# Optimization experiments

Measured on AMD Instinct MI355X. Metric: run time of the kernel, lower is better.

Reference implementation:

```python
import jax, jax.numpy as jnp
import numpy as np

B, S, D, H = 8, 1024, 1024, 16
HD = D // H  # head_dim = 64


def setup_inputs() -> dict:
    key = jax.random.key(0)
    ks = jax.random.split(key, 5)
    scale = 1.0 / np.sqrt(D)
    return {
        "x": jax.random.normal(ks[0], (B, S, D), dtype=jnp.float32),
        "wq": jax.random.normal(ks[1], (D, D), dtype=jnp.float32) * scale,
        "wk": jax.random.normal(ks[2], (D, D), dtype=jnp.float32) * scale,
        "wv": jax.random.normal(ks[3], (D, D), dtype=jnp.float32) * scale,
        "wo": jax.random.normal(ks[4], (D, D), dtype=jnp.float32) * scale,
    }


def reference(x, wq, wk, wv, wo):
    b, s, d = x.shape
    # nn.Linear: y = x @ W.T  (weights stored [out, in])
    q = (x @ wq.T).reshape(b, s, H, HD).transpose(0, 2, 1, 3)  # [b,h,s,hd]
    k = (x @ wk.T).reshape(b, s, H, HD).transpose(0, 2, 1, 3)
    v = (x @ wv.T).reshape(b, s, H, HD).transpose(0, 2, 1, 3)
    scores = jnp.einsum("bhqd,bhkd->bhqk", q, k) / jnp.sqrt(jnp.float32(HD))
    attn = jax.nn.softmax(scores, axis=-1)  # dropout p=0.0 -> identity
    out = jnp.einsum("bhqk,bhkd->bhqd", attn, v)
    out = out.transpose(0, 2, 1, 3).reshape(b, s, d)
    return out @ wo.T
```

## Files before the change

kernel.cpp:

```cpp
#include <hip/hip_runtime.h>
#include <hip/hip_bf16.h>
#include <math.h>

#define BB 8
#define SS 1024
#define DD 1024
#define HH 16
#define HDIM 64
#define MM (BB * SS)
#define QSCALE 0.1803368801111204f

typedef __attribute__((ext_vector_type(8))) short s8v;
typedef __attribute__((ext_vector_type(4))) short s4v;
typedef __attribute__((ext_vector_type(4))) float f4v;

#define GLD16(g, l)                                                            \
  __builtin_amdgcn_global_load_lds(                                            \
      (const __attribute__((address_space(1))) void*)(g),                      \
      (__attribute__((address_space(3))) void*)(l), 16, 0, 0)

__device__ __forceinline__ unsigned short bf16_ru(float f) {
  return (unsigned short)((__float_as_uint(f) + 0x8000u) >> 16);
}

__device__ __forceinline__ unsigned bf16_pack2(float f0, float f1) {
#if __has_builtin(__builtin_amdgcn_perm)
  unsigned a = __float_as_uint(f0) + 0x8000u;
  unsigned b = __float_as_uint(f1) + 0x8000u;
  return __builtin_amdgcn_perm(b, a, 0x07060302u);
#else
  return (unsigned)bf16_ru(f0) | ((unsigned)bf16_ru(f1) << 16);
#endif
}

__device__ __forceinline__ float fast_exp2(float x) {
  return __builtin_amdgcn_exp2f(x);
}

__global__ void cast_all(const float* __restrict__ x, const float* __restrict__ wq,
                         const float* __restrict__ wk, const float* __restrict__ wv,
                         const float* __restrict__ wo, __hip_bfloat16* __restrict__ xb,
                         __hip_bfloat16* __restrict__ wqkvb,
                         __hip_bfloat16* __restrict__ wob) {
  int blk = blockIdx.x;
  const float* src;
  __hip_bfloat16* dst;
  int base;
  if (blk < 2048) {
    src = x; dst = xb; base = blk * 4096;
  } else if (blk < 2304) {
    src = wq; dst = wqkvb; base = (blk - 2048) * 4096;
  } else if (blk < 2560) {
    src = wk; dst = wqkvb + (1 << 20); base = (blk - 2304) * 4096;
  } else if (blk < 2816) {
    src = wv; dst = wqkvb + (2 << 20); base = (blk - 2560) * 4096;
  } else {
    src = wo; dst = wob; base = (blk - 2816) * 4096;
  }
#pragma unroll
  for (int it = 0; it < 4; ++it) {
    int idx = base + it * 1024 + threadIdx.x * 4;
    float4 f = *(const float4*)&src[idx];
    *(uint2*)&dst[idx] = uint2{bf16_pack2(f.x, f.y), bf16_pack2(f.z, f.w)};
  }
}

template <int MODE>
__global__ __launch_bounds__(256, (MODE == 0 ? 4 : 3)) void gemm_bt(
    const __hip_bfloat16* __restrict__ A, const __hip_bfloat16* __restrict__ Bm,
    float* __restrict__ Cf, __hip_bfloat16* __restrict__ Qo,
    __hip_bfloat16* __restrict__ Ko, __hip_bfloat16* __restrict__ Vt) {
  __shared__ __hip_bfloat16 smem[2][128 * 64];
  __hip_bfloat16* sA = smem[0];
  __hip_bfloat16* sB = smem[1];

  const int tid = threadIdx.x;
  const int wave = tid >> 6;
  const int lane = tid & 63;
  const int l15 = lane & 15;
  const int quad = lane >> 4;
  const int c8 = lane & 7;
  const int r8 = lane >> 3;

  constexpr int GX = (MODE == 0) ? 16 : 8;
  constexpr int NWG = GX * 64;
  const int id = blockIdx.y * GX + blockIdx.x;
  const int nid = (id & 7) * (NWG / 8) + (id >> 3);
  const int m0 = (nid / GX) * 128;
  const int n0 = (nid % GX) * 128;

  const int wm = (wave >> 1) * 64;
  const int wn = (wave & 1) * 64;

  f4v acc[4][4];
#pragma unroll
  for (int i = 0; i < 4; ++i)
#pragma unroll
    for (int j = 0; j < 4; ++j) acc[i][j] = {0.f, 0.f, 0.f, 0.f};

  for (int kt = 0; kt < DD / 64; ++kt) {
    const int k0 = kt * 64;
    __syncthreads();
#pragma unroll
    for (int r = 0; r < 4; ++r) {
      int rb = r * 32 + wave * 8;
      int row = rb + r8;
      int scol = (c8 ^ (row & 7)) * 8;
      GLD16(A + (size_t)(m0 + row) * DD + k0 + scol, &sA[rb * 64]);
      GLD16(Bm + (size_t)(n0 + row) * DD + k0 + scol, &sB[rb * 64]);
    }
    __syncthreads();

#pragma unroll
    for (int kk = 0; kk < 2; ++kk) {
      s8v af[4], bf[4];
#pragma unroll
      for (int i = 0; i < 4; ++i)
        af[i] = *(const s8v*)&sA[(wm + i * 16 + l15) * 64 +
                                 (((kk * 4 + quad) ^ (l15 & 7)) * 8)];
#pragma unroll
      for (int j = 0; j < 4; ++j)
        bf[j] = *(const s8v*)&sB[(wn + j * 16 + l15) * 64 +
                                 (((kk * 4 + quad) ^ (l15 & 7)) * 8)];
#pragma unroll
      for (int i = 0; i < 4; ++i)
#pragma unroll
        for (int j = 0; j < 4; ++j)
          acc[i][j] = (MODE == 2)
                          ? __builtin_amdgcn_mfma_f32_16x16x32_bf16(af[i], bf[j],
                                                                    acc[i][j], 0, 0, 0)
                          : __builtin_amdgcn_mfma_f32_16x16x32_bf16(bf[j], af[i],
                                                                    acc[i][j], 0, 0, 0);
    }
  }

  if constexpr (MODE == 1) {
#pragma unroll
    for (int i = 0; i < 4; ++i) {
#pragma unroll
      for (int j = 0; j < 4; ++j) {
        const int s_abs = m0 + wm + i * 16 + l15;
        const int col = n0 + wn + j * 16 + quad * 4;
        float4 f4 = {acc[i][j][0], acc[i][j][1], acc[i][j][2], acc[i][j][3]};
        *(float4*)&Cf[(size_t)s_abs * DD + col] = f4;
      }
    }
  } else {
    __syncthreads();
    char* epc = (char*)smem + wave * 8192;
    const float scl = (MODE == 0) ? ((n0 < 1024) ? QSCALE : 1.0f) : 1.0f;
#pragma unroll
    for (int i = 0; i < 4; ++i) {
#pragma unroll
      for (int j = 0; j < 4; ++j) {
        const int r = (MODE == 0 ? i : j) * 16 + l15;
        const int c0 = (MODE == 0 ? j : i) * 16 + quad * 4;
        const int off = r * 128 + (((c0 >> 3) ^ (r & 7)) << 4) + ((c0 & 7) * 2);
        *(uint2*)(epc + off) =
            uint2{bf16_pack2(acc[i][j][0] * scl, acc[i][j][1] * scl),
                  bf16_pack2(acc[i][j][2] * scl, acc[i][j][3] * scl)};
      }
    }
    asm volatile("s_waitcnt lgkmcnt(0)" ::: "memory");
    const int rr8 = lane >> 3;
    const int ch = (lane & 7) ^ rr8;
    if constexpr (MODE == 0) {
      const bool isQ = (n0 < 1024);
      const int h = ((n0 + wn) & 1023) >> 6;
      const int sb = m0 + wm;
      const int b = sb >> 10, s0 = sb & 1023;
      __hip_bfloat16* dst =
          (isQ ? Qo : Ko) + ((size_t)(b * HH + h) * SS + s0) * HDIM;
#pragma unroll
      for (int it = 0; it < 8; ++it) {
        const int r = it * 8 + rr8;
        uint4 vv = *(const uint4*)(epc + r * 128 + ch * 16);
        *(uint4*)&dst[(size_t)r * HDIM + (lane & 7) * 8] = vv;
      }
    } else {
      const int h = ((n0 + wn) & 1023) >> 6;
      const int sb = m0 + wm;
      const int b = sb >> 10, s0 = sb & 1023;
      __hip_bfloat16* dst = Vt + (size_t)(b * HH + h) * HDIM * SS + s0;
#pragma unroll
      for (int it = 0; it < 8; ++it) {
        const int r = it * 8 + rr8;
        uint4 vv = *(const uint4*)(epc + r * 128 + ch * 16);
        *(uint4*)&dst[(size_t)r * SS + (lane & 7) * 8] = vv;
      }
    }
  }
}

#define KPLD 80
__global__ __launch_bounds__(256, 4) void attn_kernel(
    const __hip_bfloat16* __restrict__ Q, const __hip_bfloat16* __restrict__ K,
    const __hip_bfloat16* __restrict__ Vt, __hip_bfloat16* __restrict__ Oout) {
  __shared__ __hip_bfloat16 sK[64 * 64];
  __shared__ __hip_bfloat16 sVt[64 * 64];
  __shared__ unsigned short sP[4 * 32 * KPLD];

  const int tid = threadIdx.x;
  const int wave = tid >> 6;
  const int lane = tid & 63;
  const int l15 = lane & 15;
  const int quad = lane >> 4;
  const int c8 = lane & 7;
  const int r8 = lane >> 3;

  const int bh = blockIdx.x;
  const int q0 = blockIdx.y * 128;
  const size_t head = (size_t)bh * SS * HDIM;

  unsigned short* sPw = &sP[wave * 32 * KPLD];

  s8v qf[2][2];
#pragma unroll
  for (int mf = 0; mf < 2; ++mf) {
    int s = q0 + wave * 32 + mf * 16 + l15;
#pragma unroll
    for (int kk = 0; kk < 2; ++kk)
      qf[mf][kk] = *(const s8v*)&Q[head + (size_t)s * HDIM + kk * 32 + quad * 8];
  }

  s8v onesB;
#pragma unroll
  for (int j = 0; j < 8; ++j) onesB[j] = (short)0x3F80;

  f4v o[2][4];
  f4v lacc[2];
#pragma unroll
  for (int mf = 0; mf < 2; ++mf) {
    lacc[mf] = {0.f, 0.f, 0.f, 0.f};
#pragma unroll
    for (int f = 0; f < 4; ++f) o[mf][f] = {0.f, 0.f, 0.f, 0.f};
  }

  for (int kb = 0; kb < SS / 64; ++kb) {
    __syncthreads();
#pragma unroll
    for (int r = 0; r < 2; ++r) {
      int rb = r * 32 + wave * 8;
      int row = rb + r8;
      int sc8 = (c8 ^ (row & 7)) * 8;
      GLD16(&K[head + (size_t)(kb * 64 + row) * HDIM + sc8], &sK[rb * 64]);
      GLD16(&Vt[head + (size_t)row * SS + kb * 64 + sc8], &sVt[rb * 64]);
    }
    __syncthreads();

    f4v sc[2][4];
#pragma unroll
    for (int mf = 0; mf < 2; ++mf)
#pragma unroll
      for (int f = 0; f < 4; ++f) sc[mf][f] = {0.f, 0.f, 0.f, 0.f};
    __builtin_amdgcn_s_setprio(1);
#pragma unroll
    for (int kk = 0; kk < 2; ++kk) {
#pragma unroll
      for (int f = 0; f < 4; ++f) {
        s8v kf = *(const s8v*)&sK[(f * 16 + l15) * 64 +
                                  (((kk * 4 + quad) ^ (l15 & 7)) * 8)];
#pragma unroll
        for (int mf = 0; mf < 2; ++mf)
          sc[mf][f] =
              __builtin_amdgcn_mfma_f32_16x16x32_bf16(kf, qf[mf][kk], sc[mf][f], 0, 0, 0);
      }
    }
    __builtin_amdgcn_s_setprio(0);

#pragma unroll
    for (int mf = 0; mf < 2; ++mf)
#pragma unroll
      for (int f = 0; f < 4; ++f) {
        float p0 = fast_exp2(sc[mf][f][0]), p1 = fast_exp2(sc[mf][f][1]);
        float p2 = fast_exp2(sc[mf][f][2]), p3 = fast_exp2(sc[mf][f][3]);
        *(uint2*)&sPw[(mf * 16 + l15) * KPLD + f * 16 + quad * 4] =
            uint2{bf16_pack2(p0, p1), bf16_pack2(p2, p3)};
      }

    __builtin_amdgcn_s_setprio(1);
#pragma unroll
    for (int kk = 0; kk < 2; ++kk) {
      s8v pf[2];
#pragma unroll
      for (int mf = 0; mf < 2; ++mf) {
        pf[mf] = *(const s8v*)&sPw[(mf * 16 + l15) * KPLD + kk * 32 + quad * 8];
        lacc[mf] = __builtin_amdgcn_mfma_f32_16x16x32_bf16(pf[mf], onesB, lacc[mf], 0, 0, 0);
      }
#pragma unroll
      for (int f = 0; f < 4; ++f) {
        s8v vf = *(const s8v*)&sVt[(f * 16 + l15) * 64 +
                                   (((kk * 4 + quad) ^ (l15 & 7)) * 8)];
#pragma unroll
        for (int mf = 0; mf < 2; ++mf)
          o[mf][f] =
              __builtin_amdgcn_mfma_f32_16x16x32_bf16(pf[mf], vf, o[mf][f], 0, 0, 0);
      }
    }
    __builtin_amdgcn_s_setprio(0);
  }

  const int b = bh >> 4, h = bh & 15;
#pragma unroll
  for (int mf = 0; mf < 2; ++mf) {
    float rl[4];
#pragma unroll
    for (int r = 0; r < 4; ++r) rl[r] = 1.0f / lacc[mf][r];
#pragma unroll
    for (int f = 0; f < 4; ++f)
#pragma unroll
      for (int r = 0; r < 4; ++r) {
        int srow = q0 + wave * 32 + mf * 16 + quad * 4 + r;
        int col = h * HDIM + f * 16 + l15;
        ((unsigned short*)Oout)[(size_t)(b * SS + srow) * DD + col] =
            bf16_ru(o[mf][f][r] * rl[r]);
      }
  }
}

extern "C" void kernel_launch(void* const* d_in, const int* in_sizes, int n_in,
                              void* d_out, int out_size, void* d_ws, size_t ws_size,
                              hipStream_t stream) {
  const float* x = (const float*)d_in[0];
  const float* wq = (const float*)d_in[1];
  const float* wk = (const float*)d_in[2];
  const float* wv = (const float*)d_in[3];
  const float* wo = (const float*)d_in[4];

  char* ws = (char*)d_ws;
  __hip_bfloat16* xb = (__hip_bfloat16*)(ws);
  __hip_bfloat16* wqkvb = (__hip_bfloat16*)(ws + (16 << 20));
  __hip_bfloat16* wob = (__hip_bfloat16*)(ws + (22 << 20));
  __hip_bfloat16* qh = (__hip_bfloat16*)(ws + (24 << 20));
  __hip_bfloat16* kh = (__hip_bfloat16*)(ws + (40 << 20));
  __hip_bfloat16* vt = (__hip_bfloat16*)(ws + (56 << 20));
  __hip_bfloat16* attnO = (__hip_bfloat16*)(ws + (72 << 20));

  cast_all<<<3072, 256, 0, stream>>>(x, wq, wk, wv, wo, xb, wqkvb, wob);

  gemm_bt<0><<<dim3(16, 64), 256, 0, stream>>>(xb, wqkvb, nullptr, qh, kh, nullptr);
  gemm_bt<2><<<dim3(8, 64), 256, 0, stream>>>(xb, wqkvb + (2 << 20), nullptr,
                                              nullptr, nullptr, vt);

  attn_kernel<<<dim3(BB * HH, SS / 128), 256, 0, stream>>>(qh, kh, vt, attnO);

  gemm_bt<1><<<dim3(8, 64), 256, 0, stream>>>(attnO, wob, (float*)d_out, nullptr,
                                              nullptr, nullptr);
}
```

Before: 226.1 us.

## Fuse V projection into QK GEMM launch and repad attention P buffer

Result: slower. 598.4 us (+164.7%).

```diff
diff --git a/kernel.cpp b/kernel.cpp
--- a/kernel.cpp
+++ b/kernel.cpp
@@ -82,7 +82,7 @@
   const int c8 = lane & 7;
   const int r8 = lane >> 3;
 
-  constexpr int GX = (MODE == 0) ? 16 : 8;
+  constexpr int GX = (MODE == 0) ? 24 : 8;
   constexpr int NWG = GX * 64;
   const int id = blockIdx.y * GX + blockIdx.x;
   const int nid = (id & 7) * (NWG / 8) + (id >> 3);
@@ -91,6 +91,8 @@
 
   const int wm = (wave >> 1) * 64;
   const int wn = (wave & 1) * 64;
+
+  const bool noswap = (MODE == 0) && (n0 >= 2048);
 
   f4v acc[4][4];
 #pragma unroll
@@ -122,15 +124,21 @@
       for (int j = 0; j < 4; ++j)
         bf[j] = *(const s8v*)&sB[(wn + j * 16 + l15) * 64 +
                                  (((kk * 4 + quad) ^ (l15 & 7)) * 8)];
-#pragma unroll
-      for (int i = 0; i < 4; ++i)
-#pragma unroll
-        for (int j = 0; j < 4; ++j)
-          acc[i][j] = (MODE == 2)
-                          ? __builtin_amdgcn_mfma_f32_16x16x32_bf16(af[i], bf[j],
-                                                                    acc[i][j], 0, 0, 0)
-                          : __builtin_amdgcn_mfma_f32_16x16x32_bf16(bf[j], af[i],
-                                                                    acc[i][j], 0, 0, 0);
+      if (noswap) {
+#pragma unroll
+        for (int i = 0; i < 4; ++i)
+#pragma unroll
+          for (int j = 0; j < 4; ++j)
+            acc[i][j] = __builtin_amdgcn_mfma_f32_16x16x32_bf16(af[i], bf[j],
+                                                                acc[i][j], 0, 0, 0);
+      } else {
+#pragma unroll
+        for (int i = 0; i < 4; ++i)
+#pragma unroll
+          for (int j = 0; j < 4; ++j)
+            acc[i][j] = __builtin_amdgcn_mfma_f32_16x16x32_bf16(bf[j], af[i],
+                                                                acc[i][j], 0, 0, 0);
+      }
     }
   }
 
@@ -148,13 +156,14 @@
   } else {
     __syncthreads();
     char* epc = (char*)smem + wave * 8192;
-    const float scl = (MODE == 0) ? ((n0 < 1024) ? QSCALE : 1.0f) : 1.0f;
+    const bool isV = (n0 >= 2048);
+    const float scl = (n0 < 1024) ? QSCALE : 1.0f;
 #pragma unroll
     for (int i = 0; i < 4; ++i) {
 #pragma unroll
       for (int j = 0; j < 4; ++j) {
-        const int r = (MODE == 0 ? i : j) * 16 + l15;
-        const int c0 = (MODE == 0 ? j : i) * 16 + quad * 4;
+        const int r = (isV ? j : i) * 16 + l15;
+        const int c0 = (isV ? i : j) * 16 + quad * 4;
         const int off = r * 128 + (((c0 >> 3) ^ (r & 7)) << 4) + ((c0 & 7) * 2);
         *(uint2*)(epc + off) =
             uint2{bf16_pack2(acc[i][j][0] * scl, acc[i][j][1] * scl),
@@ -164,13 +173,12 @@
     asm volatile("s_waitcnt lgkmcnt(0)" ::: "memory");
     const int rr8 = lane >> 3;
     const int ch = (lane & 7) ^ rr8;
-    if constexpr (MODE == 0) {
-      const bool isQ = (n0 < 1024);
-      const int h = ((n0 + wn) & 1023) >> 6;
-      const int sb = m0 + wm;
-      const int b = sb >> 10, s0 = sb & 1023;
+    const int h = ((n0 + wn) & 1023) >> 6;
+    const int sb = m0 + wm;
+    const int b = sb >> 10, s0 = sb & 1023;
+    if (!isV) {
       __hip_bfloat16* dst =
-          (isQ ? Qo : Ko) + ((size_t)(b * HH + h) * SS + s0) * HDIM;
+          ((n0 < 1024) ? Qo : Ko) + ((size_t)(b * HH + h) * SS + s0) * HDIM;
 #pragma unroll
       for (int it = 0; it < 8; ++it) {
         const int r = it * 8 + rr8;
@@ -178,9 +186,6 @@
         *(uint4*)&dst[(size_t)r * HDIM + (lane & 7) * 8] = vv;
       }
     } else {
-      const int h = ((n0 + wn) & 1023) >> 6;
-      const int sb = m0 + wm;
-      const int b = sb >> 10, s0 = sb & 1023;
       __hip_bfloat16* dst = Vt + (size_t)(b * HH + h) * HDIM * SS + s0;
 #pragma unroll
       for (int it = 0; it < 8; ++it) {
@@ -192,7 +197,7 @@
   }
 }
 
-#define KPLD 80
+#define KPLD 76
 __global__ __launch_bounds__(256, 4) void attn_kernel(
     const __hip_bfloat16* __restrict__ Q, const __hip_bfloat16* __restrict__ K,
     const __hip_bfloat16* __restrict__ Vt, __hip_bfloat16* __restrict__ Oout) {
@@ -284,7 +289,10 @@
       s8v pf[2];
 #pragma unroll
       for (int mf = 0; mf < 2; ++mf) {
-        pf[mf] = *(const s8v*)&sPw[(mf * 16 + l15) * KPLD + kk * 32 + quad * 8];
+        const unsigned short* p = &sPw[(mf * 16 + l15) * KPLD + kk * 32 + quad * 8];
+        s4v lo = *(const s4v*)p;
+        s4v hi = *(const s4v*)(p + 4);
+        pf[mf] = __builtin_shufflevector(lo, hi, 0, 1, 2, 3, 4, 5, 6, 7);
         lacc[mf] = __builtin_amdgcn_mfma_f32_16x16x32_bf16(pf[mf], onesB, lacc[mf], 0, 0, 0);
       }
 #pragma unroll
@@ -338,9 +346,7 @@
 
   cast_all<<<3072, 256, 0, stream>>>(x, wq, wk, wv, wo, xb, wqkvb, wob);
 
-  gemm_bt<0><<<dim3(16, 64), 256, 0, stream>>>(xb, wqkvb, nullptr, qh, kh, nullptr);
-  gemm_bt<2><<<dim3(8, 64), 256, 0, stream>>>(xb, wqkvb + (2 << 20), nullptr,
-                                              nullptr, nullptr, vt);
+  gemm_bt<0><<<dim3(24, 64), 256, 0, stream>>>(xb, wqkvb, nullptr, qh, kh, vt);
 
   attn_kernel<<<dim3(BB * HH, SS / 128), 256, 0, stream>>>(qh, kh, vt, attnO);
 
```
